# Optimization experiments

Measured on AMD Instinct MI355X. Metric: run time of the kernel, lower is better.

## Reference

```python
import jax, jax.numpy as jnp
import numpy as np

B, T, D = 2, 2048, 2048
H, KVH = 32, 8
HD = D // H            # 64
G = H // KVH           # 4


def setup_inputs() -> dict:
    key = jax.random.key(0)
    k1, k2, k3 = jax.random.split(key, 3)
    x_q = jax.random.normal(k1, (B, T, D), dtype=jnp.float32)
    W_qkv = jax.random.normal(k2, (D, H * HD + 2 * KVH * HD), dtype=jnp.float32) * 0.02
    W_out = jax.random.normal(k3, (D, D), dtype=jnp.float32) * 0.02
    b_out = jnp.zeros((D,), dtype=jnp.float32)
    # real rotary tables: theta = 10000^{-2i/HD}
    inv_freq = 1.0 / (10000.0 ** (np.arange(0, HD, 2) / HD))   # [HD/2]
    pos = np.arange(T)[:, None] * inv_freq[None, :]            # [T, HD/2]
    rope_cos = jnp.asarray(np.cos(pos), dtype=jnp.float32)
    rope_sin = jnp.asarray(np.sin(pos), dtype=jnp.float32)
    return {"x_q": x_q, "W_qkv": W_qkv, "W_out": W_out, "b_out": b_out,
            "rope_cos": rope_cos, "rope_sin": rope_sin}


def _apply_rope(x, cos, sin):
    # x: [B, h, T, HD], cos/sin: [T, HD/2] -> interleaved even/odd rotation
    xe = x[..., 0::2]
    xo = x[..., 1::2]
    c = cos[None, None, :, :]
    s = sin[None, None, :, :]
    return jnp.stack([xe * c - xo * s, xe * s + xo * c], axis=-1).reshape(x.shape)


def reference(x_q, W_qkv, W_out, b_out, rope_cos, rope_sin):
    b, t, d = x_q.shape
    qkv = x_q @ W_qkv                                  # [B,T,3072]
    q_lin = qkv[..., : H * HD]
    k_lin = qkv[..., H * HD: H * HD + KVH * HD]
    v_lin = qkv[..., H * HD + KVH * HD:]
    q = q_lin.reshape(b, t, H, HD).transpose(0, 2, 1, 3)        # [B,H,T,HD]
    k = k_lin.reshape(b, t, KVH, HD).transpose(0, 2, 1, 3)      # [B,KVH,T,HD]
    v = v_lin.reshape(b, t, KVH, HD).transpose(0, 2, 1, 3)
    # GQA expand (repeat_interleave over heads)
    k = jnp.repeat(k, G, axis=1)                                # [B,H,T,HD]
    v = jnp.repeat(v, G, axis=1)
    q = _apply_rope(q, rope_cos[:t], rope_sin[:t])
    k = _apply_rope(k, rope_cos[:t], rope_sin[:t])
    scale = 1.0 / jnp.sqrt(jnp.asarray(HD, dtype=x_q.dtype))
    logits = jnp.einsum('bhqd,bhkd->bhqk', q, k) * scale        # [B,H,T,T]
    causal = jnp.triu(jnp.ones((t, t), dtype=bool), 1)[None, None]
    logits = jnp.where(causal, jnp.finfo(logits.dtype).min, logits)
    attn = jax.nn.softmax(logits, axis=-1)
    out = jnp.einsum('bhqk,bhkd->bhqd', attn, v)                # [B,H,T,HD]
    out = out.transpose(0, 2, 1, 3).reshape(b, t, H * HD)       # [B,T,D]
    out = out @ W_out + b_out
    return jnp.nan_to_num(out, nan=0.0, posinf=1e4, neginf=-1e4)
```

## Files before the change

### kernel.cpp

```cpp
#include <hip/hip_runtime.h>
#include <hip/hip_bf16.h>

#define DI __device__ __forceinline__

#if __has_builtin(__builtin_amdgcn_exp2f)
#define EXP2(x) __builtin_amdgcn_exp2f(x)
#else
#define EXP2(x) exp2f(x)
#endif

namespace {

constexpr int Bc = 2, Tc = 2048, Dc = 2048, Hc = 32, KVHc = 8, HDc = 64;
constexpr int NQKV = Hc * HDc + 2 * KVHc * HDc;

typedef __bf16 bf16x8 __attribute__((ext_vector_type(8)));
typedef unsigned short u16x8 __attribute__((ext_vector_type(8)));
typedef unsigned short u16x4 __attribute__((ext_vector_type(4)));
typedef float f32x4 __attribute__((ext_vector_type(4)));

union FragU { u16x8 u; bf16x8 b; u16x4 h[2]; };

DI float bits2f(unsigned int u) {
  union { unsigned int i; float f; } v; v.i = u << 16; return v.f;
}
DI unsigned short f2bits(float f) {
  __hip_bfloat16 h = __float2bfloat16(f);
  return *reinterpret_cast<unsigned short*>(&h);
}

DI void store_out(float* p, float v) { *p = v; }
DI void store_out(__hip_bfloat16* p, float v) { *p = __float2bfloat16(v); }

typedef __attribute__((address_space(1))) void gv_t;
typedef __attribute__((address_space(3))) void lv_t;

template<int ROWB, int TOTB, bool SWZ = false>
DI void stage_tile(const char* g, long long row_stride_b, char* lds) {
  const int tid = threadIdx.x;
  const int wid = tid >> 6, lane = tid & 63;
#pragma unroll
  for (int it = 0; it < TOTB / 4096; ++it) {
    int off = it * 4096 + wid * 1024 + lane * 16;
    int row = off / ROWB;
    int colb = off % ROWB;
    if (SWZ) colb ^= (row & 7) << 4;
    const char* gp = g + (long long)row * row_stride_b + colb;
    char* lp = lds + it * 4096 + wid * 1024;
    __builtin_amdgcn_global_load_lds((gv_t*)gp, (lv_t*)lp, 16, 0, 0);
  }
}

template<int TOTB>
DI void stage512(const char* g, long long row_stride_b, char* lds) {
  const int tid = threadIdx.x;
  const int wid = tid >> 6, lane = tid & 63;
#pragma unroll
  for (int it = 0; it < TOTB / 8192; ++it) {
    const int off = it * 8192 + wid * 1024 + lane * 16;
    const int row = off >> 7;
    const int colb = (off & 127) ^ ((row & 7) << 4);
    const char* gp = g + (long long)row * row_stride_b + colb;
    char* lp = lds + it * 8192 + wid * 1024;
    __builtin_amdgcn_global_load_lds((gv_t*)gp, (lv_t*)lp, 16, 0, 0);
  }
}

__global__ __launch_bounds__(256) void cvt_f32_bf16(
    const float* __restrict__ in, __hip_bfloat16* __restrict__ out) {
  const long long i = ((long long)blockIdx.x * 256 + threadIdx.x) * 8;
  const float4 a = *(const float4*)(in + i);
  const float4 b = *(const float4*)(in + i + 4);
  u16x8 r;
  r[0] = f2bits(a.x); r[1] = f2bits(a.y); r[2] = f2bits(a.z); r[3] = f2bits(a.w);
  r[4] = f2bits(b.x); r[5] = f2bits(b.y); r[6] = f2bits(b.z); r[7] = f2bits(b.w);
  *(u16x8*)((unsigned short*)out + i) = r;
}

__global__ __launch_bounds__(256) void transpose_cvt_kernel(
    const float* __restrict__ in, __hip_bfloat16* __restrict__ out, int R, int C) {
  __shared__ unsigned short tile[64][65];
  const int c0 = blockIdx.x * 64, r0 = blockIdx.y * 64;
  const int tid = threadIdx.x;
  const int rr = tid >> 2, seg = (tid & 3) * 16;
  const float* src = in + (long long)(r0 + rr) * C + c0 + seg;
#pragma unroll
  for (int i = 0; i < 16; ++i) tile[rr][seg + i] = f2bits(src[i]);
  __syncthreads();
  unsigned short* dst = (unsigned short*)out + (long long)(c0 + rr) * R + r0 + seg;
#pragma unroll
  for (int i = 0; i < 16; ++i) dst[i] = tile[seg + i][rr];
}

__global__ __launch_bounds__(256) void transpose_kernel(
    const __hip_bfloat16* __restrict__ in, __hip_bfloat16* __restrict__ out,
    int R, int C) {
  __shared__ unsigned short tile[64][65];
  const long long slice = (long long)R * C;
  const unsigned short* ip = (const unsigned short*)in + (long long)blockIdx.z * slice;
  unsigned short* op = (unsigned short*)out + (long long)blockIdx.z * slice;
  const int c0 = blockIdx.x * 64, r0 = blockIdx.y * 64;
  const int tid = threadIdx.x;
  const int rr = tid >> 2, seg = (tid & 3) * 16;
  const unsigned short* src = ip + (long long)(r0 + rr) * C + c0 + seg;
#pragma unroll
  for (int i = 0; i < 16; ++i) tile[rr][seg + i] = src[i];
  __syncthreads();
  unsigned short* dst = op + (long long)(c0 + rr) * R + r0 + seg;
#pragma unroll
  for (int i = 0; i < 16; ++i) dst[i] = tile[seg + i][rr];
}

template <typename OT>
__global__ __launch_bounds__(256) void gemm_bt(
    const __hip_bfloat16* __restrict__ A, const __hip_bfloat16* __restrict__ Bt,
    const float* __restrict__ bias, OT* __restrict__ C, int M, int N, int K) {
  __shared__ __align__(16) char As[2][8192];
  __shared__ __align__(16) char Bs[2][8192];
  const int nwgx = N >> 7;
  const int nwg = nwgx * (M >> 7);
  const int bid0 = blockIdx.y * nwgx + blockIdx.x;
  const int cpx = nwg >> 3;
  const int bid = (bid0 & 7) * cpx + (bid0 >> 3);
  const int n0 = (bid % nwgx) * 128;
  const int m0 = (bid / nwgx) * 128;
  const int tid = threadIdx.x;
  const int wid = tid >> 6, lane = tid & 63;
  const int wm = (wid >> 1) * 64, wn = (wid & 1) * 64;
  const int l15 = lane & 15, quad = lane >> 4;

  const char* Ag = (const char*)(A + (long long)m0 * K);
  const char* Bg = (const char*)(Bt + (long long)n0 * K);
  const long long strb = (long long)K * 2;

  f32x4 acc[4][4] = {};
  const int nk = K >> 5;

  stage_tile<64, 8192>(Ag, strb, As[0]);
  stage_tile<64, 8192>(Bg, strb, Bs[0]);
  stage_tile<64, 8192>(Ag + 64, strb, As[1]);
  stage_tile<64, 8192>(Bg + 64, strb, Bs[1]);

  for (int kt = 0; kt < nk; ++kt) {
    if (kt < nk - 1) asm volatile("s_waitcnt vmcnt(4)" ::: "memory");
    else             asm volatile("s_waitcnt vmcnt(0)" ::: "memory");
    __builtin_amdgcn_sched_barrier(0);
    __builtin_amdgcn_s_barrier();
    __builtin_amdgcn_sched_barrier(0);

    const char* as = As[kt & 1];
    const char* bs = Bs[kt & 1];
    FragU a[4], b[4];
#pragma unroll
    for (int mt = 0; mt < 4; ++mt)
      a[mt].u = *(const u16x8*)(as + ((wm + mt * 16 + l15) * 32 + quad * 8) * 2);
#pragma unroll
    for (int nt = 0; nt < 4; ++nt)
      b[nt].u = *(const u16x8*)(bs + ((wn + nt * 16 + l15) * 32 + quad * 8) * 2);
#pragma unroll
    for (int mt = 0; mt < 4; ++mt)
#pragma unroll
      for (int nt = 0; nt < 4; ++nt)
        acc[mt][nt] =
            __builtin_amdgcn_mfma_f32_16x16x32_bf16(a[mt].b, b[nt].b, acc[mt][nt], 0, 0, 0);

    __builtin_amdgcn_sched_barrier(0);
    __builtin_amdgcn_s_barrier();
    __builtin_amdgcn_sched_barrier(0);
    if (kt + 2 < nk) {
      stage_tile<64, 8192>(Ag + (long long)(kt + 2) * 64, strb, As[kt & 1]);
      stage_tile<64, 8192>(Bg + (long long)(kt + 2) * 64, strb, Bs[kt & 1]);
    }
  }

#pragma unroll
  for (int nt = 0; nt < 4; ++nt) {
    const int col = n0 + wn + nt * 16 + l15;
    const float bv = bias ? bias[col] : 0.f;
#pragma unroll
    for (int mt = 0; mt < 4; ++mt) {
#pragma unroll
      for (int r = 0; r < 4; ++r) {
        const int row = m0 + wm + mt * 16 + quad * 4 + r;
        store_out(C + (long long)row * N + col, acc[mt][nt][r] + bv);
      }
    }
  }
}

__global__ __launch_bounds__(384) void rope_reshape(
    const __hip_bfloat16* __restrict__ qkv, const float* __restrict__ cosb,
    const float* __restrict__ sinb, __hip_bfloat16* __restrict__ Qo,
    __hip_bfloat16* __restrict__ Ko, __hip_bfloat16* __restrict__ Vo) {
  constexpr float SCL = 0.125f * 1.44269504088896f;
  const int row = blockIdx.x;
  const int b = row / Tc, t = row % Tc;
  const unsigned short* src = (const unsigned short*)qkv + (long long)row * NQKV;
  const float* cb = cosb + t * 32;
  const float* sb = sinb + t * 32;
  const int e = (int)threadIdx.x * 8;
  const u16x8 v = *(const u16x8*)(src + e);
  if (e < Hc * HDc) {
    const int hh = e >> 6, d = e & 63, ii = d >> 1;
    u16x8 r;
#pragma unroll
    for (int p = 0; p < 4; ++p) {
      const float c = cb[ii + p], s = sb[ii + p];
      const float xe = bits2f(v[2 * p]), xo = bits2f(v[2 * p + 1]);
      r[2 * p] = f2bits((xe * c - xo * s) * SCL);
      r[2 * p + 1] = f2bits((xe * s + xo * c) * SCL);
    }
    const long long idx = (((long long)b * Hc + hh) * Tc + t) * HDc + d;
    *(u16x8*)((unsigned short*)Qo + idx) = r;
  } else if (e < Hc * HDc + KVHc * HDc) {
    const int e2 = e - Hc * HDc;
    const int kh = e2 >> 6, d = e2 & 63, ii = d >> 1;
    u16x8 r;
#pragma unroll
    for (int p = 0; p < 4; ++p) {
      const float c = cb[ii + p], s = sb[ii + p];
      const float xe = bits2f(v[2 * p]), xo = bits2f(v[2 * p + 1]);
      r[2 * p] = f2bits(xe * c - xo * s);
      r[2 * p + 1] = f2bits(xe * s + xo * c);
    }
    const long long idx = (((long long)b * KVHc + kh) * Tc + t) * HDc + d;
    *(u16x8*)((unsigned short*)Ko + idx) = r;
  } else {
    const int e2 = e - (Hc * HDc + KVHc * HDc);
    const int kh = e2 >> 6, d = e2 & 63;
    const long long idx = (((long long)b * KVHc + kh) * Tc + t) * HDc + d;
    *(u16x8*)((unsigned short*)Vo + idx) = v;
  }
}


DI void mask_diag(f32x4 (&S)[4], int w4, int l15, int quad) {
#pragma unroll
  for (int nt = 0; nt < 4; ++nt)
#pragma unroll
    for (int r = 0; r < 4; ++r)
      if ((nt * 16 + quad * 4 + r) > (w4 * 16 + l15)) S[nt][r] = -1e30f;
}

DI float softmax_pack(f32x4 (&S)[4], float& m_i, float& l_i, FragU (&pa)[2]) {
  float mx = fmaxf(fmaxf(S[0][0], S[0][1]), fmaxf(S[0][2], S[0][3]));
#pragma unroll
  for (int nt = 1; nt < 4; ++nt)
    mx = fmaxf(mx, fmaxf(fmaxf(S[nt][0], S[nt][1]), fmaxf(S[nt][2], S[nt][3])));
  mx = fmaxf(mx, __shfl_xor(mx, 16, 64));
  mx = fmaxf(mx, __shfl_xor(mx, 32, 64));
  const float mnew = fmaxf(m_i, mx);
  const float alpha = EXP2(m_i - mnew);
  m_i = mnew;
  float sum = 0.f;
#pragma unroll
  for (int nt = 0; nt < 4; ++nt)
#pragma unroll
    for (int r = 0; r < 4; ++r) {
      const float pp = EXP2(S[nt][r] - mnew);
      S[nt][r] = pp;
      sum += pp;
    }
  sum += __shfl_xor(sum, 16, 64);
  sum += __shfl_xor(sum, 32, 64);
  l_i = l_i * alpha + sum;
#pragma unroll
  for (int ks = 0; ks < 2; ++ks)
#pragma unroll
    for (int r = 0; r < 4; ++r) {
      pa[ks].u[r] = f2bits(S[2 * ks][r]);
      pa[ks].u[4 + r] = f2bits(S[2 * ks + 1][r]);
    }
  return alpha;
}

DI void attn_tile(const char* __restrict__ Ksb, const char* __restrict__ Vsb,
                  const FragU (&qa)[2], f32x4 (&O)[4], float& m_i, float& l_i,
                  bool diag, int w4, int l15, int quad, int sw) {
  f32x4 S[4] = {};
  __builtin_amdgcn_s_setprio(1);
#pragma unroll
  for (int nt = 0; nt < 4; ++nt) {
#pragma unroll
    for (int ks = 0; ks < 2; ++ks) {
      FragU kb;
      kb.u = *(const u16x8*)(Ksb + (nt * 16 + l15) * 128 + ((((ks << 2) | quad) ^ sw) << 4));
      S[nt] = __builtin_amdgcn_mfma_f32_16x16x32_bf16(kb.b, qa[ks].b, S[nt], 0, 0, 0);
    }
  }
  __builtin_amdgcn_s_setprio(0);
  if (diag) mask_diag(S, w4, l15, quad);
  FragU pa[2];
  const float alpha = softmax_pack(S, m_i, l_i, pa);
#pragma unroll
  for (int nt = 0; nt < 4; ++nt)
#pragma unroll
    for (int r = 0; r < 4; ++r) O[nt][r] *= alpha;
  __builtin_amdgcn_s_setprio(1);
#pragma unroll
  for (int nt = 0; nt < 4; ++nt) {
    const char* vrow = Vsb + (nt * 16 + l15) * 128 + ((quad & 1) << 3);
    const int gq = quad >> 1;
#pragma unroll
    for (int ks = 0; ks < 2; ++ks) {
      FragU vb;
      vb.h[0] = *(const u16x4*)(vrow + (((ks * 4 + gq) ^ sw) << 4));
      vb.h[1] = *(const u16x4*)(vrow + (((ks * 4 + gq + 2) ^ sw) << 4));
      O[nt] = __builtin_amdgcn_mfma_f32_16x16x32_bf16(vb.b, pa[ks].b, O[nt], 0, 0, 0);
    }
  }
  __builtin_amdgcn_s_setprio(0);
}

DI void attn_tile_dual(const char* __restrict__ Ksb, const char* __restrict__ Vsb,
                       const FragU (&qaB)[2], const FragU (&qaA)[2],
                       f32x4 (&OB)[4], f32x4 (&OA)[4],
                       float& mB, float& lB, float& mA, float& lA,
                       bool diagA, int w4, int l15, int quad, int sw) {
  f32x4 SB[4] = {}, SA[4] = {};
  __builtin_amdgcn_s_setprio(1);
#pragma unroll
  for (int nt = 0; nt < 4; ++nt) {
#pragma unroll
    for (int ks = 0; ks < 2; ++ks) {
      FragU kb;
      kb.u = *(const u16x8*)(Ksb + (nt * 16 + l15) * 128 + ((((ks << 2) | quad) ^ sw) << 4));
      SB[nt] = __builtin_amdgcn_mfma_f32_16x16x32_bf16(kb.b, qaB[ks].b, SB[nt], 0, 0, 0);
      SA[nt] = __builtin_amdgcn_mfma_f32_16x16x32_bf16(kb.b, qaA[ks].b, SA[nt], 0, 0, 0);
    }
  }
  __builtin_amdgcn_s_setprio(0);
  if (diagA) mask_diag(SA, w4, l15, quad);
  FragU paB[2], paA[2];
  const float aB = softmax_pack(SB, mB, lB, paB);
  const float aA = softmax_pack(SA, mA, lA, paA);
#pragma unroll
  for (int nt = 0; nt < 4; ++nt)
#pragma unroll
    for (int r = 0; r < 4; ++r) {
      OB[nt][r] *= aB;
      OA[nt][r] *= aA;
    }
  __builtin_amdgcn_s_setprio(1);
#pragma unroll
  for (int nt = 0; nt < 4; ++nt) {
    const char* vrow = Vsb + (nt * 16 + l15) * 128 + ((quad & 1) << 3);
    const int gq = quad >> 1;
#pragma unroll
    for (int ks = 0; ks < 2; ++ks) {
      FragU vb;
      vb.h[0] = *(const u16x4*)(vrow + (((ks * 4 + gq) ^ sw) << 4));
      vb.h[1] = *(const u16x4*)(vrow + (((ks * 4 + gq + 2) ^ sw) << 4));
      OB[nt] = __builtin_amdgcn_mfma_f32_16x16x32_bf16(vb.b, paB[ks].b, OB[nt], 0, 0, 0);
      OA[nt] = __builtin_amdgcn_mfma_f32_16x16x32_bf16(vb.b, paA[ks].b, OA[nt], 0, 0, 0);
    }
  }
  __builtin_amdgcn_s_setprio(0);
}

__global__ __launch_bounds__(512, 4) void attn_kernel(
    const __hip_bfloat16* __restrict__ Q, const __hip_bfloat16* __restrict__ K,
    const __hip_bfloat16* __restrict__ Vt, __hip_bfloat16* __restrict__ Out) {
  __shared__ __align__(16) char Ks[2][8192];
  __shared__ __align__(16) char Vs[2][8192];

  const int p = blockIdx.x;
  const int h = blockIdx.y, b = blockIdx.z;
  const int kvh = h >> 2;
  const int tid = threadIdx.x, wid = tid >> 6, lane = tid & 63;
  const int w4 = wid & 3, grp = wid >> 2;
  const int l15 = lane & 15, quad = lane >> 4;
  const int sw = l15 & 7;

  const int qtA = grp ? (15 - p) : p;
  const int qtB = grp ? (16 + p) : (31 - p);
  const int jmax = 31 - p;

  const char* QgA = (const char*)(Q + (((long long)b * Hc + h) * Tc + qtA * 64) * HDc);
  const char* QgB = (const char*)(Q + (((long long)b * Hc + h) * Tc + qtB * 64) * HDc);
  const char* Kg = (const char*)(K + (((long long)b * KVHc + kvh) * Tc) * HDc);
  const char* Vg = (const char*)(Vt + (((long long)b * KVHc + kvh) * HDc) * Tc);

  FragU qaA[2], qaB[2];
#pragma unroll
  for (int ks = 0; ks < 2; ++ks) {
    const int qoff = (w4 * 16 + l15) * 128 + (((ks << 2) | quad) << 4);
    qaA[ks].u = *(const u16x8*)(QgA + qoff);
    qaB[ks].u = *(const u16x8*)(QgB + qoff);
  }

  f32x4 OA[4] = {}, OB[4] = {};
  float mA = -1e30f, lA = 0.f, mB = -1e30f, lB = 0.f;

  stage512<8192>(Kg, 128, Ks[0]);
  stage512<8192>(Vg, (long long)Tc * 2, Vs[0]);
  asm volatile("s_waitcnt vmcnt(0)" ::: "memory");
  __syncthreads();

  for (int j = 0; j <= jmax; ++j) {
    const int cur = j & 1;
    if (j < jmax) {
      stage512<8192>(Kg + (long long)(j + 1) * 8192, 128, Ks[cur ^ 1]);
      stage512<8192>(Vg + (long long)(j + 1) * 128, (long long)Tc * 2, Vs[cur ^ 1]);
    }

    if (j <= qtA) {
      attn_tile_dual(Ks[cur], Vs[cur], qaB, qaA, OB, OA, mB, lB, mA, lA,
                     j == qtA, w4, l15, quad, sw);
    } else if (j <= qtB) {
      attn_tile(Ks[cur], Vs[cur], qaB, OB, mB, lB, j == qtB, w4, l15, quad, sw);
    }

    asm volatile("s_waitcnt vmcnt(0)" ::: "memory");
    __syncthreads();
  }

  const float invA = 1.0f / lA, invB = 1.0f / lB;
  const int tA = qtA * 64 + w4 * 16 + l15;
  const int tB = qtB * 64 + w4 * 16 + l15;
  unsigned short* obA =
      (unsigned short*)Out + ((long long)b * Tc + tA) * Dc + h * 64 + quad * 4;
  unsigned short* obB =
      (unsigned short*)Out + ((long long)b * Tc + tB) * Dc + h * 64 + quad * 4;
#pragma unroll
  for (int nt = 0; nt < 4; ++nt) {
    u16x4 va, vb;
#pragma unroll
    for (int r = 0; r < 4; ++r) {
      va[r] = f2bits(OA[nt][r] * invA);
      vb[r] = f2bits(OB[nt][r] * invB);
    }
    *(u16x4*)(obA + nt * 16) = va;
    *(u16x4*)(obB + nt * 16) = vb;
  }
}

}

extern "C" void kernel_launch(void* const* d_in, const int* in_sizes, int n_in,
                              void* d_out, int out_size, void* d_ws, size_t ws_size,
                              hipStream_t stream) {
  const float* x_q  = (const float*)d_in[0];
  const float* Wqkv = (const float*)d_in[1];
  const float* Wout = (const float*)d_in[2];
  const float* bout = (const float*)d_in[3];
  const float* rc   = (const float*)d_in[4];
  const float* rs   = (const float*)d_in[5];
  float* out = (float*)d_out;

  constexpr size_t SZ_QKV   = (size_t)Bc * Tc * NQKV * 2;
  constexpr size_t SZ_XB    = (size_t)Bc * Tc * Dc * 2;
  constexpr size_t SZ_QB    = (size_t)Bc * Hc * Tc * HDc * 2;
  constexpr size_t SZ_KV    = (size_t)Bc * KVHc * Tc * HDc * 2;
  constexpr size_t SZ_AO    = (size_t)Bc * Tc * Dc * 2;
  constexpr size_t OFF_QKV   = 0;
  constexpr size_t OFF_XB    = SZ_QKV;
  constexpr size_t OFF_WQKVT = SZ_QKV + SZ_XB;
  constexpr size_t OFF_QB    = SZ_QKV;
  constexpr size_t OFF_KB    = OFF_QB + SZ_QB;
  constexpr size_t OFF_VTMP  = OFF_KB + SZ_KV;
  constexpr size_t OFF_VT    = 0;
  constexpr size_t OFF_AO    = SZ_KV;
  constexpr size_t OFF_WOUTT = OFF_AO + SZ_AO;

  char* w = (char*)d_ws;
  __hip_bfloat16* qkv   = (__hip_bfloat16*)(w + OFF_QKV);
  __hip_bfloat16* xb    = (__hip_bfloat16*)(w + OFF_XB);
  __hip_bfloat16* WqkvT = (__hip_bfloat16*)(w + OFF_WQKVT);
  __hip_bfloat16* Qb    = (__hip_bfloat16*)(w + OFF_QB);
  __hip_bfloat16* Kb    = (__hip_bfloat16*)(w + OFF_KB);
  __hip_bfloat16* Vtmp  = (__hip_bfloat16*)(w + OFF_VTMP);
  __hip_bfloat16* Vt    = (__hip_bfloat16*)(w + OFF_VT);
  __hip_bfloat16* AO    = (__hip_bfloat16*)(w + OFF_AO);
  __hip_bfloat16* WoutT = (__hip_bfloat16*)(w + OFF_WOUTT);

  cvt_f32_bf16<<<dim3((Bc * Tc * Dc) / (256 * 8)), 256, 0, stream>>>(x_q, xb);

  transpose_cvt_kernel<<<dim3(NQKV / 64, Dc / 64), 256, 0, stream>>>(Wqkv, WqkvT, Dc, NQKV);

  gemm_bt<__hip_bfloat16><<<dim3(NQKV / 128, (Bc * Tc) / 128), 256, 0, stream>>>(
      xb, WqkvT, nullptr, qkv, Bc * Tc, NQKV, Dc);

  rope_reshape<<<dim3(Bc * Tc), 384, 0, stream>>>(qkv, rc, rs, Qb, Kb, Vtmp);

  transpose_kernel<<<dim3(HDc / 64, Tc / 64, Bc * KVHc), 256, 0, stream>>>(Vtmp, Vt, Tc, HDc);

  attn_kernel<<<dim3(Tc / 256, Hc, Bc), 512, 0, stream>>>(Qb, Kb, Vt, AO);

  transpose_cvt_kernel<<<dim3(Dc / 64, Dc / 64), 256, 0, stream>>>(Wout, WoutT, Dc, Dc);

  gemm_bt<float><<<dim3(Dc / 128, (Bc * Tc) / 128), 256, 0, stream>>>(
      AO, WoutT, bout, out, Bc * Tc, Dc, Dc);
}
```

Baseline: 309.5 us.

## Fuse prep conversions, fold V transpose into rope kernel, rebalance attention tiles

Merges the x_q bf16 conversion and the W_qkv transpose-convert into one launch, using block-index ranges to pick the path. It also folds the V transpose into the rope kernel, reading V straight from the qkv buffer, so the intermediate Vtmp buffer and a separate transpose launch go away. The attention kernel's query-tile pairing changes so each block handles adjacent tile pairs (2p+grp and 31-2p-grp), which changes the causal work balance across wave groups. Workspace offsets are rearranged to match, which risks buffer aliasing mistakes.

```diff
diff --git a/kernel.cpp b/kernel.cpp
--- a/kernel.cpp
+++ b/kernel.cpp
@@ -13,6 +13,7 @@
 
 constexpr int Bc = 2, Tc = 2048, Dc = 2048, Hc = 32, KVHc = 8, HDc = 64;
 constexpr int NQKV = Hc * HDc + 2 * KVHc * HDc;
+constexpr int VOFF = Hc * HDc + KVHc * HDc;
 
 typedef __bf16 bf16x8 __attribute__((ext_vector_type(8)));
 typedef unsigned short u16x8 __attribute__((ext_vector_type(8)));
@@ -66,15 +67,31 @@
   }
 }
 
-__global__ __launch_bounds__(256) void cvt_f32_bf16(
-    const float* __restrict__ in, __hip_bfloat16* __restrict__ out) {
-  const long long i = ((long long)blockIdx.x * 256 + threadIdx.x) * 8;
-  const float4 a = *(const float4*)(in + i);
-  const float4 b = *(const float4*)(in + i + 4);
-  u16x8 r;
-  r[0] = f2bits(a.x); r[1] = f2bits(a.y); r[2] = f2bits(a.z); r[3] = f2bits(a.w);
-  r[4] = f2bits(b.x); r[5] = f2bits(b.y); r[6] = f2bits(b.z); r[7] = f2bits(b.w);
-  *(u16x8*)((unsigned short*)out + i) = r;
+__global__ __launch_bounds__(256) void prep_kernel(
+    const float* __restrict__ x_q, __hip_bfloat16* __restrict__ xb,
+    const float* __restrict__ Wqkv, __hip_bfloat16* __restrict__ WqkvT) {
+  const int tid = threadIdx.x;
+  if (blockIdx.x < 4096) {
+    const long long i = ((long long)blockIdx.x * 256 + tid) * 8;
+    const float4 a = *(const float4*)(x_q + i);
+    const float4 b = *(const float4*)(x_q + i + 4);
+    u16x8 r;
+    r[0] = f2bits(a.x); r[1] = f2bits(a.y); r[2] = f2bits(a.z); r[3] = f2bits(a.w);
+    r[4] = f2bits(b.x); r[5] = f2bits(b.y); r[6] = f2bits(b.z); r[7] = f2bits(b.w);
+    *(u16x8*)((unsigned short*)xb + i) = r;
+  } else {
+    __shared__ unsigned short tile[64][65];
+    const int bid = blockIdx.x - 4096;
+    const int c0 = (bid % (NQKV / 64)) * 64, r0 = (bid / (NQKV / 64)) * 64;
+    const int rr = tid >> 2, seg = (tid & 3) * 16;
+    const float* src = Wqkv + (long long)(r0 + rr) * NQKV + c0 + seg;
+#pragma unroll
+    for (int i = 0; i < 16; ++i) tile[rr][seg + i] = f2bits(src[i]);
+    __syncthreads();
+    unsigned short* dst = (unsigned short*)WqkvT + (long long)(c0 + rr) * Dc + r0 + seg;
+#pragma unroll
+    for (int i = 0; i < 16; ++i) dst[i] = tile[seg + i][rr];
+  }
 }
 
 __global__ __launch_bounds__(256) void transpose_cvt_kernel(
@@ -88,25 +105,6 @@
   for (int i = 0; i < 16; ++i) tile[rr][seg + i] = f2bits(src[i]);
   __syncthreads();
   unsigned short* dst = (unsigned short*)out + (long long)(c0 + rr) * R + r0 + seg;
-#pragma unroll
-  for (int i = 0; i < 16; ++i) dst[i] = tile[seg + i][rr];
-}
-
-__global__ __launch_bounds__(256) void transpose_kernel(
-    const __hip_bfloat16* __restrict__ in, __hip_bfloat16* __restrict__ out,
-    int R, int C) {
-  __shared__ unsigned short tile[64][65];
-  const long long slice = (long long)R * C;
-  const unsigned short* ip = (const unsigned short*)in + (long long)blockIdx.z * slice;
-  unsigned short* op = (unsigned short*)out + (long long)blockIdx.z * slice;
-  const int c0 = blockIdx.x * 64, r0 = blockIdx.y * 64;
-  const int tid = threadIdx.x;
-  const int rr = tid >> 2, seg = (tid & 3) * 16;
-  const unsigned short* src = ip + (long long)(r0 + rr) * C + c0 + seg;
-#pragma unroll
-  for (int i = 0; i < 16; ++i) tile[rr][seg + i] = src[i];
-  __syncthreads();
-  unsigned short* dst = op + (long long)(c0 + rr) * R + r0 + seg;
 #pragma unroll
   for (int i = 0; i < 16; ++i) dst[i] = tile[seg + i][rr];
 }
@@ -188,48 +186,66 @@
   }
 }
 
-__global__ __launch_bounds__(384) void rope_reshape(
+__global__ __launch_bounds__(384) void rope_v_kernel(
     const __hip_bfloat16* __restrict__ qkv, const float* __restrict__ cosb,
     const float* __restrict__ sinb, __hip_bfloat16* __restrict__ Qo,
-    __hip_bfloat16* __restrict__ Ko, __hip_bfloat16* __restrict__ Vo) {
+    __hip_bfloat16* __restrict__ Ko, __hip_bfloat16* __restrict__ Vt) {
   constexpr float SCL = 0.125f * 1.44269504088896f;
-  const int row = blockIdx.x;
-  const int b = row / Tc, t = row % Tc;
-  const unsigned short* src = (const unsigned short*)qkv + (long long)row * NQKV;
-  const float* cb = cosb + t * 32;
-  const float* sb = sinb + t * 32;
-  const int e = (int)threadIdx.x * 8;
-  const u16x8 v = *(const u16x8*)(src + e);
-  if (e < Hc * HDc) {
-    const int hh = e >> 6, d = e & 63, ii = d >> 1;
-    u16x8 r;
-#pragma unroll
-    for (int p = 0; p < 4; ++p) {
-      const float c = cb[ii + p], s = sb[ii + p];
-      const float xe = bits2f(v[2 * p]), xo = bits2f(v[2 * p + 1]);
-      r[2 * p] = f2bits((xe * c - xo * s) * SCL);
-      r[2 * p + 1] = f2bits((xe * s + xo * c) * SCL);
-    }
-    const long long idx = (((long long)b * Hc + hh) * Tc + t) * HDc + d;
-    *(u16x8*)((unsigned short*)Qo + idx) = r;
-  } else if (e < Hc * HDc + KVHc * HDc) {
-    const int e2 = e - Hc * HDc;
-    const int kh = e2 >> 6, d = e2 & 63, ii = d >> 1;
-    u16x8 r;
-#pragma unroll
-    for (int p = 0; p < 4; ++p) {
-      const float c = cb[ii + p], s = sb[ii + p];
-      const float xe = bits2f(v[2 * p]), xo = bits2f(v[2 * p + 1]);
-      r[2 * p] = f2bits(xe * c - xo * s);
-      r[2 * p + 1] = f2bits(xe * s + xo * c);
-    }
-    const long long idx = (((long long)b * KVHc + kh) * Tc + t) * HDc + d;
-    *(u16x8*)((unsigned short*)Ko + idx) = r;
+  const int tid = threadIdx.x;
+  if (blockIdx.x < Bc * Tc) {
+    const int row = blockIdx.x;
+    const int b = row / Tc, t = row % Tc;
+    const unsigned short* src = (const unsigned short*)qkv + (long long)row * NQKV;
+    const float* cb = cosb + t * 32;
+    const float* sb = sinb + t * 32;
+    const int e = tid * 8;
+    if (e < Hc * HDc) {
+      const u16x8 v = *(const u16x8*)(src + e);
+      const int hh = e >> 6, d = e & 63, ii = d >> 1;
+      u16x8 r;
+#pragma unroll
+      for (int p = 0; p < 4; ++p) {
+        const float c = cb[ii + p], s = sb[ii + p];
+        const float xe = bits2f(v[2 * p]), xo = bits2f(v[2 * p + 1]);
+        r[2 * p] = f2bits((xe * c - xo * s) * SCL);
+        r[2 * p + 1] = f2bits((xe * s + xo * c) * SCL);
+      }
+      const long long idx = (((long long)b * Hc + hh) * Tc + t) * HDc + d;
+      *(u16x8*)((unsigned short*)Qo + idx) = r;
+    } else if (e < VOFF) {
+      const u16x8 v = *(const u16x8*)(src + e);
+      const int e2 = e - Hc * HDc;
+      const int kh = e2 >> 6, d = e2 & 63, ii = d >> 1;
+      u16x8 r;
+#pragma unroll
+      for (int p = 0; p < 4; ++p) {
+        const float c = cb[ii + p], s = sb[ii + p];
+        const float xe = bits2f(v[2 * p]), xo = bits2f(v[2 * p + 1]);
+        r[2 * p] = f2bits(xe * c - xo * s);
+        r[2 * p + 1] = f2bits(xe * s + xo * c);
+      }
+      const long long idx = (((long long)b * KVHc + kh) * Tc + t) * HDc + d;
+      *(u16x8*)((unsigned short*)Ko + idx) = r;
+    }
   } else {
-    const int e2 = e - (Hc * HDc + KVHc * HDc);
-    const int kh = e2 >> 6, d = e2 & 63;
-    const long long idx = (((long long)b * KVHc + kh) * Tc + t) * HDc + d;
-    *(u16x8*)((unsigned short*)Vo + idx) = v;
+    __shared__ unsigned short tile[64][65];
+    const int bid = blockIdx.x - Bc * Tc;
+    const int z = bid >> 5;
+    const int b = z >> 3, kvh = z & 7;
+    const int t0 = (bid & 31) * 64;
+    const int rr = (tid & 255) >> 2, seg = (tid & 3) * 16;
+    if (tid < 256) {
+      const unsigned short* src = (const unsigned short*)qkv +
+          (long long)(b * Tc + t0 + rr) * NQKV + VOFF + kvh * 64 + seg;
+#pragma unroll
+      for (int i = 0; i < 16; ++i) tile[rr][seg + i] = src[i];
+    }
+    __syncthreads();
+    if (tid < 256) {
+      unsigned short* dst = (unsigned short*)Vt + ((long long)z * HDc + rr) * Tc + t0 + seg;
+#pragma unroll
+      for (int i = 0; i < 16; ++i) dst[i] = tile[seg + i][rr];
+    }
   }
 }
 
@@ -372,9 +388,9 @@
   const int l15 = lane & 15, quad = lane >> 4;
   const int sw = l15 & 7;
 
-  const int qtA = grp ? (15 - p) : p;
-  const int qtB = grp ? (16 + p) : (31 - p);
-  const int jmax = 31 - p;
+  const int qtA = 2 * p + grp;
+  const int qtB = 31 - 2 * p - grp;
+  const int jmax = 31 - 2 * p;
 
   const char* QgA = (const char*)(Q + (((long long)b * Hc + h) * Tc + qtA * 64) * HDc);
   const char* QgB = (const char*)(Q + (((long long)b * Hc + h) * Tc + qtB * 64) * HDc);
@@ -450,16 +466,14 @@
 
   constexpr size_t SZ_QKV   = (size_t)Bc * Tc * NQKV * 2;
   constexpr size_t SZ_XB    = (size_t)Bc * Tc * Dc * 2;
-  constexpr size_t SZ_QB    = (size_t)Bc * Hc * Tc * HDc * 2;
   constexpr size_t SZ_KV    = (size_t)Bc * KVHc * Tc * HDc * 2;
   constexpr size_t SZ_AO    = (size_t)Bc * Tc * Dc * 2;
   constexpr size_t OFF_QKV   = 0;
   constexpr size_t OFF_XB    = SZ_QKV;
   constexpr size_t OFF_WQKVT = SZ_QKV + SZ_XB;
   constexpr size_t OFF_QB    = SZ_QKV;
-  constexpr size_t OFF_KB    = OFF_QB + SZ_QB;
-  constexpr size_t OFF_VTMP  = OFF_KB + SZ_KV;
-  constexpr size_t OFF_VT    = 0;
+  constexpr size_t OFF_KB    = OFF_WQKVT;
+  constexpr size_t OFF_VT    = OFF_KB + SZ_KV;
   constexpr size_t OFF_AO    = SZ_KV;
   constexpr size_t OFF_WOUTT = OFF_AO + SZ_AO;
 
@@ -469,21 +483,18 @@
   __hip_bfloat16* WqkvT = (__hip_bfloat16*)(w + OFF_WQKVT);
   __hip_bfloat16* Qb    = (__hip_bfloat16*)(w + OFF_QB);
   __hip_bfloat16* Kb    = (__hip_bfloat16*)(w + OFF_KB);
-  __hip_bfloat16* Vtmp  = (__hip_bfloat16*)(w + OFF_VTMP);
   __hip_bfloat16* Vt    = (__hip_bfloat16*)(w + OFF_VT);
   __hip_bfloat16* AO    = (__hip_bfloat16*)(w + OFF_AO);
   __hip_bfloat16* WoutT = (__hip_bfloat16*)(w + OFF_WOUTT);
 
-  cvt_f32_bf16<<<dim3((Bc * Tc * Dc) / (256 * 8)), 256, 0, stream>>>(x_q, xb);
-
-  transpose_cvt_kernel<<<dim3(NQKV / 64, Dc / 64), 256, 0, stream>>>(Wqkv, WqkvT, Dc, NQKV);
+  prep_kernel<<<dim3(4096 + (NQKV / 64) * (Dc / 64)), 256, 0, stream>>>(
+      x_q, xb, Wqkv, WqkvT);
 
   gemm_bt<__hip_bfloat16><<<dim3(NQKV / 128, (Bc * Tc) / 128), 256, 0, stream>>>(
       xb, WqkvT, nullptr, qkv, Bc * Tc, NQKV, Dc);
 
-  rope_reshape<<<dim3(Bc * Tc), 384, 0, stream>>>(qkv, rc, rs, Qb, Kb, Vtmp);
-
-  transpose_kernel<<<dim3(HDc / 64, Tc / 64, Bc * KVHc), 256, 0, stream>>>(Vtmp, Vt, Tc, HDc);
+  rope_v_kernel<<<dim3(Bc * Tc + Bc * KVHc * (Tc / 64)), 384, 0, stream>>>(
+      qkv, rc, rs, Qb, Kb, Vt);
 
   attn_kernel<<<dim3(Tc / 256, Hc, Bc), 512, 0, stream>>>(Qb, Kb, Vt, AO);
 
```

Result: no change. 305.9 us (-1.1%).
